# Optimization experiments

Measured on AMD Instinct MI355X. Metric: run time of the kernel, lower is better.

## Reference

```python
import jax, jax.numpy as jnp
import numpy as np

TOTAL = 16777216  # total jagged values
SEGS = 8192       # number of segments (prefix_sum length)


def setup_inputs() -> dict:
    key = jax.random.key(0)
    k1, k2 = jax.random.split(key)
    logits = jax.random.normal(k1, (TOTAL,), dtype=jnp.float32)
    prefix_sum = jnp.sort(jax.random.randint(k2, (SEGS,), 0, TOTAL, dtype=jnp.int32))
    # prefix_sum holds cumulative (exclusive) segment end offsets; last must equal TOTAL
    prefix_sum = prefix_sum.at[-1].set(TOTAL)
    return {"logits": logits, "prefix_sum": prefix_sum}


def reference(logits, prefix_sum):
    n = logits.shape[0]
    num_segs = prefix_sum.shape[0]
    # element i belongs to segment j where prefix_sum[j-1] <= i < prefix_sum[j]
    seg = jnp.searchsorted(prefix_sum, jnp.arange(n, dtype=prefix_sum.dtype), side="right")
    # numerically stable per-segment log-softmax
    seg_max = jax.ops.segment_max(logits, seg, num_segments=num_segs)
    shifted = logits - seg_max[seg]
    seg_sumexp = jax.ops.segment_sum(jnp.exp(shifted), seg, num_segments=num_segs)
    return shifted - jnp.log(seg_sumexp)[seg]
```

## Files before the change

### kernel.cpp

```cpp
#include <hip/hip_runtime.h>
#include <math.h>

#define TPB 256

__global__ __launch_bounds__(TPB) void jls_kernel(
    const float* __restrict__ x,
    const int* __restrict__ prefix,
    float* __restrict__ out)
{
    const int seg   = blockIdx.x;
    const int start = (seg == 0) ? 0 : prefix[seg - 1];
    const int end   = prefix[seg];
    if (end <= start) return;

    const int tid = threadIdx.x;

    int a0 = (start + 3) & ~3;  if (a0 > end) a0 = end;
    int a1 = end & ~3;          if (a1 < a0) a1 = a0;
    const float4* __restrict__ x4 = (const float4*)x;
    const int v0 = a0 >> 2, v1 = a1 >> 2;

    __shared__ float sbuf[4];

    float m = -INFINITY;
    for (int i = start + tid; i < a0; i += TPB) m = fmaxf(m, x[i]);
    for (int i = v0 + tid; i < v1; i += TPB) {
        float4 v = x4[i];
        m = fmaxf(m, fmaxf(fmaxf(v.x, v.y), fmaxf(v.z, v.w)));
    }
    for (int i = a1 + tid; i < end; i += TPB) m = fmaxf(m, x[i]);

    #pragma unroll
    for (int off = 32; off > 0; off >>= 1)
        m = fmaxf(m, __shfl_xor(m, off, 64));
    if ((tid & 63) == 0) sbuf[tid >> 6] = m;
    __syncthreads();
    m = fmaxf(fmaxf(sbuf[0], sbuf[1]), fmaxf(sbuf[2], sbuf[3]));
    __syncthreads();

    float l = 0.0f;
    for (int i = start + tid; i < a0; i += TPB) l += __expf(x[i] - m);
    for (int i = v0 + tid; i < v1; i += TPB) {
        float4 v = x4[i];
        l += __expf(v.x - m) + __expf(v.y - m) + __expf(v.z - m) + __expf(v.w - m);
    }
    for (int i = a1 + tid; i < end; i += TPB) l += __expf(x[i] - m);

    #pragma unroll
    for (int off = 32; off > 0; off >>= 1)
        l += __shfl_xor(l, off, 64);
    if ((tid & 63) == 0) sbuf[tid >> 6] = l;
    __syncthreads();
    l = sbuf[0] + sbuf[1] + sbuf[2] + sbuf[3];

    const float c = m + __logf(l);

    float4* __restrict__ o4 = (float4*)out;
    for (int i = start + tid; i < a0; i += TPB) out[i] = x[i] - c;
    for (int i = v0 + tid; i < v1; i += TPB) {
        float4 v = x4[i];
        float4 r;
        r.x = v.x - c; r.y = v.y - c; r.z = v.z - c; r.w = v.w - c;
        o4[i] = r;
    }
    for (int i = a1 + tid; i < end; i += TPB) out[i] = x[i] - c;
}

extern "C" void kernel_launch(void* const* d_in, const int* in_sizes, int n_in,
                              void* d_out, int out_size, void* d_ws, size_t ws_size,
                              hipStream_t stream) {
    const float* logits = (const float*)d_in[0];
    const int*   prefix = (const int*)d_in[1];
    float*       out    = (float*)d_out;
    const int num_segs  = in_sizes[1];

    jls_kernel<<<num_segs, TPB, 0, stream>>>(logits, prefix, out);
}
```

Measured before the change: 129.5 us.

## Use online softmax to fuse max and sum-exp passes into one read

Replaces the separate max pass and sum-of-exp pass with a single online-softmax pass that keeps a running max and rescaled sum per thread. The partial (max, sum) pairs are merged across the wavefront and block with a combine step. This removes one full read of each segment from global memory. It also unrolls the vector loops by two, using independent accumulators to add memory-level parallelism. The cost is extra exp and branch work whenever the running max changes.

```diff
diff --git a/kernel.cpp b/kernel.cpp
--- a/kernel.cpp
+++ b/kernel.cpp
@@ -2,6 +2,18 @@
 #include <math.h>
 
 #define TPB 256
+
+__device__ __forceinline__ float max4(float4 v) {
+    return fmaxf(fmaxf(v.x, v.y), fmaxf(v.z, v.w));
+}
+
+__device__ __forceinline__ void combine(float& m, float& l, float mo, float lo) {
+    float mn = fmaxf(m, mo);
+    float a = (l  > 0.0f) ? l  * __expf(m  - mn) : 0.0f;
+    float b = (lo > 0.0f) ? lo * __expf(mo - mn) : 0.0f;
+    m = mn;
+    l = a + b;
+}
 
 __global__ __launch_bounds__(TPB) void jls_kernel(
     const float* __restrict__ x,
@@ -20,50 +32,71 @@
     const float4* __restrict__ x4 = (const float4*)x;
     const int v0 = a0 >> 2, v1 = a1 >> 2;
 
-    __shared__ float sbuf[4];
-
-    float m = -INFINITY;
-    for (int i = start + tid; i < a0; i += TPB) m = fmaxf(m, x[i]);
-    for (int i = v0 + tid; i < v1; i += TPB) {
-        float4 v = x4[i];
-        m = fmaxf(m, fmaxf(fmaxf(v.x, v.y), fmaxf(v.z, v.w)));
+    float m0 = -INFINITY, l0 = 0.0f;
+    float m1 = -INFINITY, l1 = 0.0f;
+    int i = v0 + tid;
+    for (; i + TPB < v1; i += 2 * TPB) {
+        float4 a = x4[i];
+        float4 b = x4[i + TPB];
+        float am = max4(a), bm = max4(b);
+        if (am > m0) { l0 *= __expf(m0 - am); m0 = am; }
+        l0 += __expf(a.x - m0) + __expf(a.y - m0) + __expf(a.z - m0) + __expf(a.w - m0);
+        if (bm > m1) { l1 *= __expf(m1 - bm); m1 = bm; }
+        l1 += __expf(b.x - m1) + __expf(b.y - m1) + __expf(b.z - m1) + __expf(b.w - m1);
     }
-    for (int i = a1 + tid; i < end; i += TPB) m = fmaxf(m, x[i]);
+    if (i < v1) {
+        float4 a = x4[i];
+        float am = max4(a);
+        if (am > m0) { l0 *= __expf(m0 - am); m0 = am; }
+        l0 += __expf(a.x - m0) + __expf(a.y - m0) + __expf(a.z - m0) + __expf(a.w - m0);
+    }
+    for (int j = start + tid; j < a0; j += TPB) {
+        float v = x[j];
+        if (v > m0) { l0 *= __expf(m0 - v); m0 = v; }
+        l0 += __expf(v - m0);
+    }
+    for (int j = a1 + tid; j < end; j += TPB) {
+        float v = x[j];
+        if (v > m1) { l1 *= __expf(m1 - v); m1 = v; }
+        l1 += __expf(v - m1);
+    }
+    combine(m0, l0, m1, l1);
 
     #pragma unroll
-    for (int off = 32; off > 0; off >>= 1)
-        m = fmaxf(m, __shfl_xor(m, off, 64));
-    if ((tid & 63) == 0) sbuf[tid >> 6] = m;
+    for (int off = 32; off > 0; off >>= 1) {
+        float mo = __shfl_xor(m0, off, 64);
+        float lo = __shfl_xor(l0, off, 64);
+        combine(m0, l0, mo, lo);
+    }
+    __shared__ float sm[4], sl[4];
+    if ((tid & 63) == 0) { sm[tid >> 6] = m0; sl[tid >> 6] = l0; }
     __syncthreads();
-    m = fmaxf(fmaxf(sbuf[0], sbuf[1]), fmaxf(sbuf[2], sbuf[3]));
-    __syncthreads();
+    float M = sm[0], L = sl[0];
+    combine(M, L, sm[1], sl[1]);
+    combine(M, L, sm[2], sl[2]);
+    combine(M, L, sm[3], sl[3]);
 
-    float l = 0.0f;
-    for (int i = start + tid; i < a0; i += TPB) l += __expf(x[i] - m);
-    for (int i = v0 + tid; i < v1; i += TPB) {
-        float4 v = x4[i];
-        l += __expf(v.x - m) + __expf(v.y - m) + __expf(v.z - m) + __expf(v.w - m);
-    }
-    for (int i = a1 + tid; i < end; i += TPB) l += __expf(x[i] - m);
-
-    #pragma unroll
-    for (int off = 32; off > 0; off >>= 1)
-        l += __shfl_xor(l, off, 64);
-    if ((tid & 63) == 0) sbuf[tid >> 6] = l;
-    __syncthreads();
-    l = sbuf[0] + sbuf[1] + sbuf[2] + sbuf[3];
-
-    const float c = m + __logf(l);
+    const float c = M + __logf(L);
 
     float4* __restrict__ o4 = (float4*)out;
-    for (int i = start + tid; i < a0; i += TPB) out[i] = x[i] - c;
-    for (int i = v0 + tid; i < v1; i += TPB) {
-        float4 v = x4[i];
-        float4 r;
-        r.x = v.x - c; r.y = v.y - c; r.z = v.z - c; r.w = v.w - c;
-        o4[i] = r;
+    i = v0 + tid;
+    for (; i + TPB < v1; i += 2 * TPB) {
+        float4 a = x4[i];
+        float4 b = x4[i + TPB];
+        float4 ra, rb;
+        ra.x = a.x - c; ra.y = a.y - c; ra.z = a.z - c; ra.w = a.w - c;
+        rb.x = b.x - c; rb.y = b.y - c; rb.z = b.z - c; rb.w = b.w - c;
+        o4[i] = ra;
+        o4[i + TPB] = rb;
     }
-    for (int i = a1 + tid; i < end; i += TPB) out[i] = x[i] - c;
+    if (i < v1) {
+        float4 a = x4[i];
+        float4 ra;
+        ra.x = a.x - c; ra.y = a.y - c; ra.z = a.z - c; ra.w = a.w - c;
+        o4[i] = ra;
+    }
+    for (int j = start + tid; j < a0; j += TPB) out[j] = x[j] - c;
+    for (int j = a1 + tid;   j < end; j += TPB) out[j] = x[j] - c;
 }
 
 extern "C" void kernel_launch(void* const* d_in, const int* in_sizes, int n_in,
```

Result: faster. 120.0 us (-7.3%).
